# Kernel tuning notes

Hardware: AMD Instinct MI355X
Metric: run time of the kernel (lower is better)

Reference implementation:

```python
import jax, jax.numpy as jnp
import numpy as np

TOP_K = 10  # hard-coded k=10 in the original tf.nn.top_k call


def setup_inputs() -> dict:
    key = jax.random.key(0)
    k1, k2 = jax.random.split(key)
    x = jax.random.normal(k1, (32768, 128), dtype=jnp.float32)
    cluster_centers = jax.random.normal(k2, (512, 128), dtype=jnp.float32)
    return {"x": x, "cluster_centers": cluster_centers}


def reference(x, cluster_centers):
    # (mathematically identical to tf.norm(x[:, None, :] - centers, axis=-1)
    #  without materializing the [N, K, D] difference tensor).
    x2 = jnp.sum(x * x, axis=-1, keepdims=True)            # [N, 1]
    c2 = jnp.sum(cluster_centers * cluster_centers, -1)    # [K]
    d2 = x2 - 2.0 * (x @ cluster_centers.T) + c2           # [N, K]
    distances = jnp.sqrt(jnp.maximum(d2, 0.0))
    # top-k smallest distances -> cluster indices (values in [0, K))
    _, indices = jax.lax.top_k(-distances, TOP_K)          # [N, 10] int32
    # Faithful to the original: gather POINTS x at these cluster indices
    closest_points = x[indices]                            # [N, 10, D]
    return closest_points.reshape(1, -1, x.shape[-1])      # [1, N*10, D]
```

## Files before the change

### kernel.cpp

```cpp
#include <hip/hip_runtime.h>
#include <stdint.h>

typedef unsigned long long u64;

#define NPTS 32768
#define NCEN 512
#define DIM  128
#define TOPK 10

#define KSTEP 32
#define LDX 132
#define LDC 516
#define KPAD 81

#define SMEM_BYTES 88064

__global__ __launch_bounds__(256) void np_rownorm(const float* __restrict__ src,
                                                  float* __restrict__ dst, int nrows) {
  const int t = threadIdx.x;
  const int lane = t & 63;
  const int wv = t >> 6;
  const int g = lane >> 3;
  const int j = lane & 7;
  const int row = blockIdx.x * 32 + wv * 8 + g;
  if (row >= nrows) return;
  const float* p = src + (size_t)row * DIM;

  float v = p[j];
  float r = __fmul_rn(v, v);
#pragma unroll
  for (int b = 1; b < 16; ++b) {
    v = p[8 * b + j];
    r = __fadd_rn(r, __fmul_rn(v, v));
  }
  r = __fadd_rn(r, __shfl_xor(r, 1, 64));
  r = __fadd_rn(r, __shfl_xor(r, 2, 64));
  r = __fadd_rn(r, __shfl_xor(r, 4, 64));
  if (j == 0) dst[row] = r;
}

__global__ __launch_bounds__(1024) void fused_kernel(const float* __restrict__ x,
                                                     const float* __restrict__ cen,
                                                     const float* __restrict__ x2,
                                                     const float* __restrict__ c2,
                                                     float* __restrict__ out) {
  __shared__ __align__(16) char smem[SMEM_BYTES];
  float* xT = (float*)smem;
  float* cT = (float*)(smem + (size_t)KSTEP * LDX * 4);
  u64*  keysL   = (u64*)smem;
  unsigned* mergedL = (unsigned*)(smem + (size_t)128 * KPAD * 8);

  const int t  = threadIdx.x;
  const int pb = blockIdx.x * 128;

  const int wid  = t >> 6;
  const int lane = t & 63;
  const int wr = wid >> 3, wc = wid & 7;
  const int r = lane & 7, c = lane >> 3;
  const int px = wr * 64 + 4 * r;
  const int cx = wc * 64 + 4 * c;

  float acc[8][8];
#pragma unroll
  for (int i = 0; i < 8; ++i)
#pragma unroll
    for (int j = 0; j < 8; ++j) acc[i][j] = 0.f;

  const int xrow = t & 127, xkh = ((t >> 7) & 1) * 16;
  const int crow = t & 511, ckh = (t >> 9) * 16;

  for (int s = 0; s < DIM / KSTEP; ++s) {
    if (s) __syncthreads();
    if (t < 256) {
      const float4* srcx = (const float4*)&x[(size_t)(pb + xrow) * DIM + s * KSTEP + xkh];
#pragma unroll
      for (int i = 0; i < 4; ++i) {
        float4 v = srcx[i];
        int k = xkh + i * 4;
        xT[(k + 0) * LDX + xrow] = v.x; xT[(k + 1) * LDX + xrow] = v.y;
        xT[(k + 2) * LDX + xrow] = v.z; xT[(k + 3) * LDX + xrow] = v.w;
      }
    }
    {
      const float4* srcc = (const float4*)&cen[(size_t)crow * DIM + s * KSTEP + ckh];
#pragma unroll
      for (int i = 0; i < 4; ++i) {
        float4 v = srcc[i];
        int k = ckh + i * 4;
        cT[(k + 0) * LDC + crow] = v.x; cT[(k + 1) * LDC + crow] = v.y;
        cT[(k + 2) * LDC + crow] = v.z; cT[(k + 3) * LDC + crow] = v.w;
      }
    }
    __syncthreads();

#pragma unroll 4
    for (int kk = 0; kk < KSTEP; ++kk) {
      float4 xa  = *(const float4*)&xT[kk * LDX + px];
      float4 xb  = *(const float4*)&xT[kk * LDX + px + 32];
      float4 ca  = *(const float4*)&cT[kk * LDC + cx];
      float4 cb2 = *(const float4*)&cT[kk * LDC + cx + 32];
      float xv[8] = {xa.x, xa.y, xa.z, xa.w, xb.x, xb.y, xb.z, xb.w};
      float cv[8] = {ca.x, ca.y, ca.z, ca.w, cb2.x, cb2.y, cb2.z, cb2.w};
#pragma unroll
      for (int i = 0; i < 8; ++i)
#pragma unroll
        for (int j = 0; j < 8; ++j)
          acc[i][j] = __fmaf_rn(xv[i], cv[j], acc[i][j]);
    }
  }
  __syncthreads();

  const float4 cc0 = *(const float4*)&c2[cx];
  const float4 cc1 = *(const float4*)&c2[cx + 32];
#pragma unroll
  for (int i = 0; i < 8; ++i) {
    const int pt = px + (i & 3) + (i >> 2) * 32;
    const float xx = x2[pb + pt];
    u64 key[8];
#pragma unroll
    for (int jq = 0; jq < 2; ++jq) {
      const float4 cc = jq ? cc1 : cc0;
      float t0 = __fmaf_rn(-2.f, acc[i][jq * 4 + 0], xx);
      float t1 = __fmaf_rn(-2.f, acc[i][jq * 4 + 1], xx);
      float t2 = __fmaf_rn(-2.f, acc[i][jq * 4 + 2], xx);
      float t3 = __fmaf_rn(-2.f, acc[i][jq * 4 + 3], xx);
      float d0 = sqrtf(fmaxf(__fadd_rn(t0, cc.x), 0.f));
      float d1 = sqrtf(fmaxf(__fadd_rn(t1, cc.y), 0.f));
      float d2 = sqrtf(fmaxf(__fadd_rn(t2, cc.z), 0.f));
      float d3 = sqrtf(fmaxf(__fadd_rn(t3, cc.w), 0.f));
      const unsigned cbase = (unsigned)(cx + 32 * jq);
      key[jq * 4 + 0] = ((u64)__float_as_uint(d0) << 32) | (cbase + 0);
      key[jq * 4 + 1] = ((u64)__float_as_uint(d1) << 32) | (cbase + 1);
      key[jq * 4 + 2] = ((u64)__float_as_uint(d2) << 32) | (cbase + 2);
      key[jq * 4 + 3] = ((u64)__float_as_uint(d3) << 32) | (cbase + 3);
    }
#pragma unroll
    for (int tt = 0; tt < TOPK; ++tt) {
      u64 m = key[0];
#pragma unroll
      for (int s2 = 1; s2 < 8; ++s2) m = (key[s2] < m) ? key[s2] : m;
      u64 o;
      o = __shfl_xor(m, 8, 64);  m = (o < m) ? o : m;
      o = __shfl_xor(m, 16, 64); m = (o < m) ? o : m;
      o = __shfl_xor(m, 32, 64); m = (o < m) ? o : m;
      if (c == 0) keysL[(size_t)pt * KPAD + wc * 10 + tt] = m;
#pragma unroll
      for (int s2 = 0; s2 < 8; ++s2)
        if (key[s2] == m) key[s2] = ~0ull;
    }
  }
  __syncthreads();

  {
    const int g  = lane >> 3;
    const int cs = lane & 7;
    const int mp = wid * 8 + g;
    int ptr = 0;
#pragma unroll
    for (int tt = 0; tt < TOPK; ++tt) {
      u64 head = (ptr < 10) ? keysL[(size_t)mp * KPAD + cs * 10 + ptr] : ~0ull;
      u64 m = head;
      u64 o;
      o = __shfl_xor(m, 1, 64); m = (o < m) ? o : m;
      o = __shfl_xor(m, 2, 64); m = (o < m) ? o : m;
      o = __shfl_xor(m, 4, 64); m = (o < m) ? o : m;
      if (head == m) ptr++;
      if (cs == 0) mergedL[mp * 10 + tt] = (unsigned)(m & 0x1ffu);
    }
  }
  __syncthreads();

  {
    const int p0 = wid * 8;
#pragma unroll
    for (int pp = 0; pp < 8; ++pp) {
#pragma unroll
      for (int tt = 0; tt < TOPK; ++tt) {
        const int idx = mergedL[(p0 + pp) * 10 + tt];
        const float2 v = *(const float2*)&x[(size_t)idx * DIM + 2 * lane];
        *(float2*)&out[(((size_t)(pb + p0 + pp)) * TOPK + tt) * DIM + 2 * lane] = v;
      }
    }
  }
}

extern "C" void kernel_launch(void* const* d_in, const int* in_sizes, int n_in,
                              void* d_out, int out_size, void* d_ws, size_t ws_size,
                              hipStream_t stream) {
  const float* x   = (const float*)d_in[0];
  const float* cen = (const float*)d_in[1];
  float* out = (float*)d_out;

  float* c2 = (float*)d_ws;
  float* x2 = (float*)((char*)d_ws + 4096);

  np_rownorm<<<NCEN / 32, 256, 0, stream>>>(cen, c2, NCEN);
  np_rownorm<<<NPTS / 32, 256, 0, stream>>>(x, x2, NPTS);
  fused_kernel<<<NPTS / 128, 1024, 0, stream>>>(x, cen, x2, c2, out);
}
```

Baseline: 135.7 us.

## Split fused kernel into tiled GEMM-select and separate merge-gather kernels

The single 1024-thread fused kernel, which processed all 512 centers per block of 128 points, becomes a 2D-grid GEMM kernel over 128x128 tiles with 256 threads and a smaller shared-memory footprint, aiming for higher occupancy and more blocks. Each tile writes per-64-center partial top-10 keys to a global workspace, and a new per-point wave kernel merges the 80 candidates and gathers the output rows. The two row-norm launches are also merged into one. The cost is an extra kernel launch and global traffic for the intermediate keys, about 21 MB written and read back.

```diff
diff --git a/kernel.cpp b/kernel.cpp
--- a/kernel.cpp
+++ b/kernel.cpp
@@ -8,23 +8,29 @@
 #define DIM  128
 #define TOPK 10
 
+#define BM 128
+#define BN 128
 #define KSTEP 32
-#define LDX 132
-#define LDC 516
-#define KPAD 81
-
-#define SMEM_BYTES 88064
-
-__global__ __launch_bounds__(256) void np_rownorm(const float* __restrict__ src,
-                                                  float* __restrict__ dst, int nrows) {
+#define LDT 132
+#define KP 21
+
+#define SMEM1 33792
+
+__global__ __launch_bounds__(256) void np_rownorm_all(const float* __restrict__ x,
+                                                      const float* __restrict__ cen,
+                                                      float* __restrict__ x2,
+                                                      float* __restrict__ c2) {
   const int t = threadIdx.x;
   const int lane = t & 63;
   const int wv = t >> 6;
   const int g = lane >> 3;
   const int j = lane & 7;
   const int row = blockIdx.x * 32 + wv * 8 + g;
-  if (row >= nrows) return;
-  const float* p = src + (size_t)row * DIM;
+  if (row >= NCEN + NPTS) return;
+  const float* p;
+  float* dst;
+  if (row < NCEN) { p = cen + (size_t)row * DIM; dst = c2 + row; }
+  else            { p = x + (size_t)(row - NCEN) * DIM; dst = x2 + (row - NCEN); }
 
   float v = p[j];
   float r = __fmul_rn(v, v);
@@ -36,26 +42,29 @@
   r = __fadd_rn(r, __shfl_xor(r, 1, 64));
   r = __fadd_rn(r, __shfl_xor(r, 2, 64));
   r = __fadd_rn(r, __shfl_xor(r, 4, 64));
-  if (j == 0) dst[row] = r;
-}
-
-__global__ __launch_bounds__(1024) void fused_kernel(const float* __restrict__ x,
-                                                     const float* __restrict__ cen,
-                                                     const float* __restrict__ x2,
-                                                     const float* __restrict__ c2,
-                                                     float* __restrict__ out) {
-  __shared__ __align__(16) char smem[SMEM_BYTES];
+  if (j == 0) *dst = r;
+}
+
+__global__ __launch_bounds__(256, 4) void gemm_select_kernel(const float* __restrict__ x,
+                                                             const float* __restrict__ cen,
+                                                             const float* __restrict__ x2,
+                                                             const float* __restrict__ c2,
+                                                             u64* __restrict__ keysG) {
+  __shared__ __align__(16) char smem[SMEM1];
   float* xT = (float*)smem;
-  float* cT = (float*)(smem + (size_t)KSTEP * LDX * 4);
-  u64*  keysL   = (u64*)smem;
-  unsigned* mergedL = (unsigned*)(smem + (size_t)128 * KPAD * 8);
+  float* cT = (float*)(smem + 16896);
+  u64*  keysL = (u64*)smem;
 
   const int t  = threadIdx.x;
-  const int pb = blockIdx.x * 128;
+  const int pb = blockIdx.y * BM;
+  const int cb = blockIdx.x * BN;
+
+  const int srow = t & 127;
+  const int kh   = (t >> 7) * 16;
 
   const int wid  = t >> 6;
   const int lane = t & 63;
-  const int wr = wid >> 3, wc = wid & 7;
+  const int wr = wid >> 1, wc = wid & 1;
   const int r = lane & 7, c = lane >> 3;
   const int px = wr * 64 + 4 * r;
   const int cx = wc * 64 + 4 * c;
@@ -66,39 +75,34 @@
 #pragma unroll
     for (int j = 0; j < 8; ++j) acc[i][j] = 0.f;
 
-  const int xrow = t & 127, xkh = ((t >> 7) & 1) * 16;
-  const int crow = t & 511, ckh = (t >> 9) * 16;
-
   for (int s = 0; s < DIM / KSTEP; ++s) {
     if (s) __syncthreads();
-    if (t < 256) {
-      const float4* srcx = (const float4*)&x[(size_t)(pb + xrow) * DIM + s * KSTEP + xkh];
+    {
+      const float4* srcx = (const float4*)&x[(size_t)(pb + srow) * DIM + s * KSTEP + kh];
+      const float4* srcc = (const float4*)&cen[(size_t)(cb + srow) * DIM + s * KSTEP + kh];
 #pragma unroll
       for (int i = 0; i < 4; ++i) {
         float4 v = srcx[i];
-        int k = xkh + i * 4;
-        xT[(k + 0) * LDX + xrow] = v.x; xT[(k + 1) * LDX + xrow] = v.y;
-        xT[(k + 2) * LDX + xrow] = v.z; xT[(k + 3) * LDX + xrow] = v.w;
+        int k = kh + i * 4;
+        xT[(k + 0) * LDT + srow] = v.x; xT[(k + 1) * LDT + srow] = v.y;
+        xT[(k + 2) * LDT + srow] = v.z; xT[(k + 3) * LDT + srow] = v.w;
       }
-    }
-    {
-      const float4* srcc = (const float4*)&cen[(size_t)crow * DIM + s * KSTEP + ckh];
 #pragma unroll
       for (int i = 0; i < 4; ++i) {
         float4 v = srcc[i];
-        int k = ckh + i * 4;
-        cT[(k + 0) * LDC + crow] = v.x; cT[(k + 1) * LDC + crow] = v.y;
-        cT[(k + 2) * LDC + crow] = v.z; cT[(k + 3) * LDC + crow] = v.w;
+        int k = kh + i * 4;
+        cT[(k + 0) * LDT + srow] = v.x; cT[(k + 1) * LDT + srow] = v.y;
+        cT[(k + 2) * LDT + srow] = v.z; cT[(k + 3) * LDT + srow] = v.w;
       }
     }
     __syncthreads();
 
 #pragma unroll 4
     for (int kk = 0; kk < KSTEP; ++kk) {
-      float4 xa  = *(const float4*)&xT[kk * LDX + px];
-      float4 xb  = *(const float4*)&xT[kk * LDX + px + 32];
-      float4 ca  = *(const float4*)&cT[kk * LDC + cx];
-      float4 cb2 = *(const float4*)&cT[kk * LDC + cx + 32];
+      float4 xa  = *(const float4*)&xT[kk * LDT + px];
+      float4 xb  = *(const float4*)&xT[kk * LDT + px + 32];
+      float4 ca  = *(const float4*)&cT[kk * LDT + cx];
+      float4 cb2 = *(const float4*)&cT[kk * LDT + cx + 32];
       float xv[8] = {xa.x, xa.y, xa.z, xa.w, xb.x, xb.y, xb.z, xb.w};
       float cv[8] = {ca.x, ca.y, ca.z, ca.w, cb2.x, cb2.y, cb2.z, cb2.w};
 #pragma unroll
@@ -110,8 +114,8 @@
   }
   __syncthreads();
 
-  const float4 cc0 = *(const float4*)&c2[cx];
-  const float4 cc1 = *(const float4*)&c2[cx + 32];
+  const float4 cc0 = *(const float4*)&c2[cb + cx];
+  const float4 cc1 = *(const float4*)&c2[cb + cx + 32];
 #pragma unroll
   for (int i = 0; i < 8; ++i) {
     const int pt = px + (i & 3) + (i >> 2) * 32;
@@ -128,7 +132,7 @@
       float d1 = sqrtf(fmaxf(__fadd_rn(t1, cc.y), 0.f));
       float d2 = sqrtf(fmaxf(__fadd_rn(t2, cc.z), 0.f));
       float d3 = sqrtf(fmaxf(__fadd_rn(t3, cc.w), 0.f));
-      const unsigned cbase = (unsigned)(cx + 32 * jq);
+      const unsigned cbase = (unsigned)(cb + cx + 32 * jq);
       key[jq * 4 + 0] = ((u64)__float_as_uint(d0) << 32) | (cbase + 0);
       key[jq * 4 + 1] = ((u64)__float_as_uint(d1) << 32) | (cbase + 1);
       key[jq * 4 + 2] = ((u64)__float_as_uint(d2) << 32) | (cbase + 2);
@@ -143,7 +147,7 @@
       o = __shfl_xor(m, 8, 64);  m = (o < m) ? o : m;
       o = __shfl_xor(m, 16, 64); m = (o < m) ? o : m;
       o = __shfl_xor(m, 32, 64); m = (o < m) ? o : m;
-      if (c == 0) keysL[(size_t)pt * KPAD + wc * 10 + tt] = m;
+      if (c == 0) keysL[pt * KP + wc * 10 + tt] = m;
 #pragma unroll
       for (int s2 = 0; s2 < 8; ++s2)
         if (key[s2] == m) key[s2] = ~0ull;
@@ -152,35 +156,42 @@
   __syncthreads();
 
   {
-    const int g  = lane >> 3;
-    const int cs = lane & 7;
-    const int mp = wid * 8 + g;
-    int ptr = 0;
-#pragma unroll
-    for (int tt = 0; tt < TOPK; ++tt) {
-      u64 head = (ptr < 10) ? keysL[(size_t)mp * KPAD + cs * 10 + ptr] : ~0ull;
-      u64 m = head;
-      u64 o;
-      o = __shfl_xor(m, 1, 64); m = (o < m) ? o : m;
-      o = __shfl_xor(m, 2, 64); m = (o < m) ? o : m;
-      o = __shfl_xor(m, 4, 64); m = (o < m) ? o : m;
-      if (head == m) ptr++;
-      if (cs == 0) mergedL[mp * 10 + tt] = (unsigned)(m & 0x1ffu);
-    }
-  }
-  __syncthreads();
-
-  {
-    const int p0 = wid * 8;
-#pragma unroll
-    for (int pp = 0; pp < 8; ++pp) {
-#pragma unroll
-      for (int tt = 0; tt < TOPK; ++tt) {
-        const int idx = mergedL[(p0 + pp) * 10 + tt];
-        const float2 v = *(const float2*)&x[(size_t)idx * DIM + 2 * lane];
-        *(float2*)&out[(((size_t)(pb + p0 + pp)) * TOPK + tt) * DIM + 2 * lane] = v;
-      }
-    }
+    const int p = t >> 1, half = t & 1;
+    const u64* srcL = &keysL[p * KP + half * 10];
+    u64* dst = &keysG[(size_t)(pb + p) * 80 + (cb >> 6) * 10 + half * 10];
+#pragma unroll
+    for (int q = 0; q < 10; ++q) dst[q] = srcL[q];
+  }
+}
+
+__global__ __launch_bounds__(256) void merge_gather_kernel(const u64* __restrict__ keysG,
+                                                           const float* __restrict__ x,
+                                                           float* __restrict__ out) {
+  const int p    = blockIdx.x * 4 + (threadIdx.x >> 6);
+  const int lane = threadIdx.x & 63;
+
+  const u64* kp = keysG + (size_t)p * 80;
+  u64 ka = kp[lane];
+  u64 kb = (lane < 16) ? kp[64 + lane] : ~0ull;
+
+  float* op = out + (size_t)p * TOPK * DIM;
+  int ptr = 0;
+
+#pragma unroll
+  for (int tt = 0; tt < TOPK; ++tt) {
+    const int src = lane * 10 + ptr;
+    u64 ha = __shfl(ka, src, 64);
+    u64 hb = __shfl(kb, (src >= 64) ? (src - 64) : 0, 64);
+    u64 head = (lane < 8 && ptr < 10) ? ((src < 64) ? ha : hb) : ~0ull;
+    u64 m = head, o;
+    o = __shfl_xor(m, 1, 64); m = (o < m) ? o : m;
+    o = __shfl_xor(m, 2, 64); m = (o < m) ? o : m;
+    o = __shfl_xor(m, 4, 64); m = (o < m) ? o : m;
+    m = __shfl(m, 0, 64);
+    if (head == m) ptr++;
+    const int idx = (int)(m & 0x1ffull);
+    const float2 v = *(const float2*)&x[(size_t)idx * DIM + 2 * lane];
+    *(float2*)&op[tt * DIM + 2 * lane] = v;
   }
 }
 
@@ -193,8 +204,9 @@
 
   float* c2 = (float*)d_ws;
   float* x2 = (float*)((char*)d_ws + 4096);
-
-  np_rownorm<<<NCEN / 32, 256, 0, stream>>>(cen, c2, NCEN);
-  np_rownorm<<<NPTS / 32, 256, 0, stream>>>(x, x2, NPTS);
-  fused_kernel<<<NPTS / 128, 1024, 0, stream>>>(x, cen, x2, c2, out);
-}
+  u64* keys = (u64*)((char*)d_ws + 4096 + 131072);
+
+  np_rownorm_all<<<(NCEN + NPTS) / 32, 256, 0, stream>>>(x, cen, x2, c2);
+  gemm_select_kernel<<<dim3(NCEN / BN, NPTS / BM), 256, 0, stream>>>(x, cen, x2, c2, keys);
+  merge_gather_kernel<<<NPTS / 4, 256, 0, stream>>>(keys, x, out);
+}
```

Measured after the change: 154.2 us. 13.6% more time.
